# Optimization experiments

Measured on AMD Instinct MI355X. Metric: run time of the kernel, lower is better.

## Reference

```python
import jax, jax.numpy as jnp
import numpy as np

B, S, D, H, F = 4, 2048, 256, 8, 2  # batch, seq, input_size, heads, mlp factor
EPS = 1e-5


def _ln(x, g, b):
    m = jnp.mean(x, axis=-1, keepdims=True)
    v = jnp.var(x, axis=-1, keepdims=True)
    return (x - m) / jnp.sqrt(v + EPS) * g + b


def setup_inputs() -> dict:
    key = jax.random.key(0)
    ks = jax.random.split(key, 12)
    s = 1.0 / np.sqrt(D)
    return {
        "X":  jax.random.normal(ks[0], (B, S, D), jnp.float32),
        # Wide attention: each of H heads has full [D,D] Q/K/V projections (no bias)
        "Wq": jax.random.uniform(ks[1], (H, D, D), jnp.float32, -s, s),
        "Wk": jax.random.uniform(ks[2], (H, D, D), jnp.float32, -s, s),
        "Wv": jax.random.uniform(ks[3], (H, D, D), jnp.float32, -s, s),
        "Wz": jax.random.uniform(ks[4], (H * D, D), jnp.float32, -1.0 / np.sqrt(H * D), 1.0 / np.sqrt(H * D)),
        "bz": jnp.zeros((D,), jnp.float32),
        "W1": jax.random.uniform(ks[5], (D, F * D), jnp.float32, -s, s),
        "b1": jnp.zeros((F * D,), jnp.float32),
        "W2": jax.random.uniform(ks[6], (F * D, D), jnp.float32, -1.0 / np.sqrt(F * D), 1.0 / np.sqrt(F * D)),
        "b2": jnp.zeros((D,), jnp.float32),
        "g1": jnp.ones((D,), jnp.float32),
        "be1": jnp.zeros((D,), jnp.float32),
        "g2": jnp.ones((D,), jnp.float32),
        "be2": jnp.zeros((D,), jnp.float32),
    }


def reference(X, Wq, Wk, Wv, Wz, bz, W1, b1, W2, b2, g1, be1, g2, be2):
    scale = D ** (-0.25)  # applied to both q and k as in the source
    q = jnp.einsum('bsd,hde->hbse', X, Wq) * scale   # [H,B,S,D]
    k = jnp.einsum('btd,hde->hbte', X, Wk) * scale
    v = jnp.einsum('btd,hde->hbte', X, Wv)
    attn = jax.nn.softmax(jnp.einsum('hbse,hbte->hbst', q, k), axis=-1)  # [H,B,S,S]
    zh = jnp.einsum('hbst,hbte->hbse', attn, v)       # [H,B,S,D]
    # concat heads along feature dim (head order matters for Wz)
    zcat = jnp.transpose(zh, (1, 2, 0, 3)).reshape(B, S, H * D)
    z = zcat @ Wz + bz
    z = _ln(z + X, g1, be1)                            # dropout p=0 -> identity
    z_ff = jnp.maximum(z @ W1 + b1, 0.0) @ W2 + b2
    z = _ln(z_ff + z, g2, be2)
    attn_mean = jnp.mean(attn, axis=0)                 # [B,S,S]
    return z, attn_mean
```

## Files before the change

### kernel.cpp

```cpp
#include <hip/hip_runtime.h>
#include <cstdint>
#include <cstddef>

#define B_  4
#define S_  2048
#define D_  256
#define H_  8
#define FD_ 512
#define N_  (B_*S_)
#define HD_ (H_*D_)
#define EPS 1e-5f

typedef __attribute__((ext_vector_type(8))) short bf16x8;
typedef __attribute__((ext_vector_type(8))) unsigned short u16x8;
typedef __attribute__((ext_vector_type(4))) float f32x4;

__device__ __forceinline__ unsigned short f2bf(float f) {
  union { float f; unsigned u; } x; x.f = f;
  unsigned u = x.u;
  return (unsigned short)((u + 0x7FFFu + ((u >> 16) & 1u)) >> 16);
}
__device__ __forceinline__ float bf2f(unsigned short h) {
  union { unsigned u; float f; } x; x.u = ((unsigned)h) << 16; return x.f;
}

__device__ __forceinline__ void glds16(const void* gptr, void* ldsptr) {
  __builtin_amdgcn_global_load_lds(
      (__attribute__((address_space(1))) void*)gptr,
      (__attribute__((address_space(3))) void*)ldsptr,
      16, 0, 0);
}

__device__ __forceinline__ int sw32(int row, int u) {
  return (row*32 + ((u & 24) | ((u & 7) ^ (row & 7)))) * 8;
}
__device__ __forceinline__ int sw16(int row, int u) {
  return (row*16 + ((u & 8) | ((u & 7) ^ (row & 7)))) * 8;
}

__global__ __launch_bounds__(256) void cast_x_kernel(
    const float* __restrict__ X, unsigned short* __restrict__ Xb)
{
  const size_t i8 = ((size_t)blockIdx.x * 256 + threadIdx.x) * 8;
  float4 a = *(const float4*)&X[i8];
  float4 b = *(const float4*)&X[i8 + 4];
  u16x8 o;
  o[0]=f2bf(a.x); o[1]=f2bf(a.y); o[2]=f2bf(a.z); o[3]=f2bf(a.w);
  o[4]=f2bf(b.x); o[5]=f2bf(b.y); o[6]=f2bf(b.z); o[7]=f2bf(b.w);
  *(u16x8*)&Xb[i8] = o;
}

__global__ __launch_bounds__(256) void prep_w_kernel(
    const float* __restrict__ Wq, const float* __restrict__ Wk,
    const float* __restrict__ Wv, unsigned short* __restrict__ Wt)
{
  __shared__ float tile[64][65];
  const int tid = threadIdx.x;
  const int d0 = blockIdx.x * 64, e0 = blockIdx.y * 64;
  const int w = blockIdx.z;
  const float* src;
  float scale;
  if (w < 8)       { src = Wq + (size_t)w*D_*D_;      scale = 0.25f; }
  else if (w < 16) { src = Wk + (size_t)(w-8)*D_*D_;  scale = 0.25f; }
  else             { src = Wv + (size_t)(w-16)*D_*D_; scale = 1.0f;  }
  {
    int r = tid >> 2, c16 = (tid & 3) * 16;
    const float* s = src + (size_t)(d0 + r)*D_ + e0 + c16;
    #pragma unroll
    for (int u = 0; u < 4; ++u) *(float4*)&tile[r][c16 + u*4] = *(const float4*)(s + u*4);
  }
  __syncthreads();
  {
    int er = tid >> 2, dc = (tid & 3) * 16;
    u16x8 o0, o1;
    #pragma unroll
    for (int j = 0; j < 8; ++j) {
      o0[j] = f2bf(tile[dc + j][er] * scale);
      o1[j] = f2bf(tile[dc + 8 + j][er] * scale);
    }
    unsigned short* dst = Wt + ((size_t)w*D_ + e0 + er)*D_ + d0 + dc;
    *(u16x8*)(dst)     = o0;
    *(u16x8*)(dst + 8) = o1;
  }
}

__global__ __launch_bounds__(256) void tcast_kernel(
    const float* __restrict__ src, unsigned short* __restrict__ dst,
    int R, int C)
{
  __shared__ float tile[64][65];
  const int tid = threadIdx.x;
  const int r0 = blockIdx.x * 64, c0 = blockIdx.y * 64;
  {
    int r = tid >> 2, c16 = (tid & 3) * 16;
    const float* s = src + (size_t)(r0 + r)*C + c0 + c16;
    #pragma unroll
    for (int u = 0; u < 4; ++u) *(float4*)&tile[r][c16 + u*4] = *(const float4*)(s + u*4);
  }
  __syncthreads();
  {
    int cr = tid >> 2, rc = (tid & 3) * 16;
    u16x8 o0, o1;
    #pragma unroll
    for (int j = 0; j < 8; ++j) {
      o0[j] = f2bf(tile[rc + j][cr]);
      o1[j] = f2bf(tile[rc + 8 + j][cr]);
    }
    unsigned short* d = dst + (size_t)(c0 + cr)*R + r0 + rc;
    *(u16x8*)(d)     = o0;
    *(u16x8*)(d + 8) = o1;
  }
}

__global__ __launch_bounds__(256) void qkv_kernel(
    const unsigned short* __restrict__ Xb, const unsigned short* __restrict__ Wt,
    unsigned short* __restrict__ q, unsigned short* __restrict__ k,
    unsigned short* __restrict__ v)
{
  __shared__ unsigned short Xt[64*32*8];
  __shared__ unsigned short Wtile[64*32*8];
  const int tid = threadIdx.x;
  const int w4 = tid >> 6, lane = tid & 63;
  const int c = lane & 15, qd = lane >> 4;
  const int n0 = blockIdx.x * 64;
  const int e0 = blockIdx.y * 64;
  const int w  = blockIdx.z;

  unsigned short* obase;
  if (w < 8)       obase = q + (size_t)w*N_*D_;
  else if (w < 16) obase = k + (size_t)(w-8)*N_*D_;
  else             obase = v + (size_t)(w-16)*N_*D_;

  {
    const char* xg = (const char*)Xb + (size_t)n0*512;
    const char* wg = (const char*)Wt + ((size_t)w*D_ + e0)*512;
    #pragma unroll
    for (int i = 0; i < 8; ++i) {
      int g = w4*8 + i;
      int r = 2*g + (lane >> 5);
      int su = lane & 31;
      int u = (su & 24) | ((su & 7) ^ (r & 7));
      glds16(xg + (size_t)r*512 + u*16, &Xt[g*512]);
      glds16(wg + (size_t)r*512 + u*16, &Wtile[g*512]);
    }
  }
  __syncthreads();

  f32x4 sc[4];
  #pragma unroll
  for (int nc = 0; nc < 4; ++nc) sc[nc] = (f32x4){0.f,0.f,0.f,0.f};
  #pragma unroll
  for (int ks = 0; ks < 8; ++ks) {
    bf16x8 xa = *(const bf16x8*)&Xt[sw32(16*w4 + c, ks*4 + qd)];
    #pragma unroll
    for (int nc = 0; nc < 4; ++nc) {
      bf16x8 bf = *(const bf16x8*)&Wtile[sw32(nc*16 + c, ks*4 + qd)];
      sc[nc] = __builtin_amdgcn_mfma_f32_16x16x32_bf16(xa, bf, sc[nc], 0, 0, 0);
    }
  }
  #pragma unroll
  for (int nc = 0; nc < 4; ++nc)
    #pragma unroll
    for (int r = 0; r < 4; ++r)
      obase[(size_t)(n0 + 16*w4 + qd*4 + r)*D_ + e0 + nc*16 + c] = f2bf(sc[nc][r]);
}

__global__ __launch_bounds__(256) void vtrans_kernel(
    const unsigned short* __restrict__ vb, unsigned short* __restrict__ vT)
{
  __shared__ unsigned short tile[64][72];
  const int tid = threadIdx.x;
  const int t0 = blockIdx.x * 64, e0 = blockIdx.y * 64;
  const int h = blockIdx.z >> 2, b = blockIdx.z & 3;
  const size_t in_base = (size_t)h*N_*D_ + (size_t)b*S_*D_;
  {
    int r = tid >> 2, c16 = (tid & 3) * 16;
    const unsigned short* src = vb + in_base + (size_t)(t0 + r)*D_ + e0 + c16;
    *(u16x8*)&tile[r][c16]     = *(const u16x8*)(src);
    *(u16x8*)&tile[r][c16 + 8] = *(const u16x8*)(src + 8);
  }
  __syncthreads();
  {
    int er = tid >> 2, tt = (tid & 3) * 16;
    u16x8 o0, o1;
    #pragma unroll
    for (int j = 0; j < 8; ++j) { o0[j] = tile[tt+j][er]; o1[j] = tile[tt+8+j][er]; }
    unsigned short* dst = vT + ((size_t)(h*4 + b)*D_ + e0 + er)*S_ + t0 + tt;
    *(u16x8*)(dst)     = o0;
    *(u16x8*)(dst + 8) = o1;
  }
}

__global__ __launch_bounds__(256, 2) void attn_ol_kernel(
    const unsigned short* __restrict__ qb, const unsigned short* __restrict__ kb,
    const unsigned short* __restrict__ vT, unsigned short* __restrict__ zcatb,
    float* __restrict__ Lws)
{
  __shared__ unsigned short Kt[2][32*32*8];
  __shared__ unsigned short Vt[2][16*544];
  const int tid = threadIdx.x;
  const int w = tid >> 6, lane = tid & 63;
  const int c = lane & 15, qd = lane >> 4;
  const int s0 = blockIdx.x * 128;
  const int b = blockIdx.y, h = blockIdx.z;

  const size_t qkbase = (size_t)h*N_*D_ + (size_t)b*S_*D_;

  bf16x8 qa[2][8];
  #pragma unroll
  for (int mi = 0; mi < 2; ++mi) {
    const unsigned short* qrow = qb + qkbase + (size_t)(s0 + 32*w + 16*mi + c)*D_ + qd*8;
    #pragma unroll
    for (int ks = 0; ks < 8; ++ks) qa[mi][ks] = *(const bf16x8*)(qrow + ks*32);
  }

  f32x4 o[2][16];
  #pragma unroll
  for (int mi = 0; mi < 2; ++mi)
    #pragma unroll
    for (int i = 0; i < 16; ++i) o[mi][i] = (f32x4){0.f,0.f,0.f,0.f};
  float Lp[2] = {0.f, 0.f};

  const char* kB = (const char*)(kb + qkbase);
  const char* vB = (const char*)(vT + (size_t)(h*4 + b)*D_*S_);

  #define STAGE_OL(kt_, bi_)                                                   \
    {                                                                          \
      _Pragma("unroll")                                                        \
      for (int i = 0; i < 4; ++i) {                                            \
        int g = w*4 + i;                                                       \
        int r = 2*g + (lane >> 5);                                             \
        int Lg = ((r >> 2) & 3)*8 + (r >> 4)*4 + (r & 3);                      \
        int su = lane & 31;                                                    \
        int u = (su & 24) | ((su & 7) ^ (r & 7));                              \
        glds16(kB + ((size_t)(kt_)*32 + Lg)*512 + u*16, &Kt[bi_][g*512]);      \
      }                                                                        \
      _Pragma("unroll")                                                        \
      for (int i = 0; i < 4; ++i) {                                            \
        int g = w*4 + i;                                                       \
        int e = g*16 + (lane >> 2);                                            \
        int qv = (lane & 3) ^ ((lane >> 3) & 3);                               \
        glds16(vB + (size_t)e*4096 + (size_t)(kt_)*64 + qv*16, &Vt[bi_][g*544]);\
      }                                                                        \
    }

  STAGE_OL(0, 0);

  for (int kt = 0; kt < 64; ++kt) {
    const int bi = kt & 1;
    __syncthreads();
    if (kt + 1 < 64) STAGE_OL(kt + 1, bi ^ 1);

    f32x4 sc[2][2];
    #pragma unroll
    for (int mi = 0; mi < 2; ++mi)
      #pragma unroll
      for (int nc = 0; nc < 2; ++nc) sc[mi][nc] = (f32x4){0.f,0.f,0.f,0.f};
    #pragma unroll
    for (int ks = 0; ks < 8; ++ks) {
      bf16x8 kf0 = *(const bf16x8*)&Kt[bi][sw32(c,      ks*4 + qd)];
      bf16x8 kf1 = *(const bf16x8*)&Kt[bi][sw32(16 + c, ks*4 + qd)];
      #pragma unroll
      for (int mi = 0; mi < 2; ++mi) {
        sc[mi][0] = __builtin_amdgcn_mfma_f32_16x16x32_bf16(kf0, qa[mi][ks], sc[mi][0], 0, 0, 0);
        sc[mi][1] = __builtin_amdgcn_mfma_f32_16x16x32_bf16(kf1, qa[mi][ks], sc[mi][1], 0, 0, 0);
      }
    }
    bf16x8 pa[2];
    #pragma unroll
    for (int mi = 0; mi < 2; ++mi) {
      float ex[2][4];
      #pragma unroll
      for (int nc = 0; nc < 2; ++nc)
        #pragma unroll
        for (int r = 0; r < 4; ++r) {
          float p = __expf(sc[mi][nc][r]);
          ex[nc][r] = p;
          Lp[mi] += p;
        }
      union { unsigned u[4]; bf16x8 v; } cv;
      asm("v_cvt_pk_bf16_f32 %0, %1, %2" : "=v"(cv.u[0]) : "v"(ex[0][0]), "v"(ex[0][1]));
      asm("v_cvt_pk_bf16_f32 %0, %1, %2" : "=v"(cv.u[1]) : "v"(ex[0][2]), "v"(ex[0][3]));
      asm("v_cvt_pk_bf16_f32 %0, %1, %2" : "=v"(cv.u[2]) : "v"(ex[1][0]), "v"(ex[1][1]));
      asm("v_cvt_pk_bf16_f32 %0, %1, %2" : "=v"(cv.u[3]) : "v"(ex[1][2]), "v"(ex[1][3]));
      pa[mi] = cv.v;
    }
    #pragma unroll
    for (int ec = 0; ec < 16; ++ec) {
      bf16x8 vf = *(const bf16x8*)&Vt[bi][ec*544 + c*32 + (qd ^ ((c >> 1) & 3))*8];
      o[0][ec] = __builtin_amdgcn_mfma_f32_16x16x32_bf16(pa[0], vf, o[0][ec], 0, 0, 0);
      o[1][ec] = __builtin_amdgcn_mfma_f32_16x16x32_bf16(pa[1], vf, o[1][ec], 0, 0, 0);
    }
  }

  #pragma unroll
  for (int mi = 0; mi < 2; ++mi) {
    float L = Lp[mi];
    L += __shfl_xor(L, 16);
    L += __shfl_xor(L, 32);
    if (qd == 0)
      Lws[(size_t)h*N_ + b*S_ + s0 + 32*w + 16*mi + c] = L;
    float il[4];
    #pragma unroll
    for (int r = 0; r < 4; ++r)
      il[r] = 1.0f / __shfl(L, (lane & 48) | (qd*4 + r));
    #pragma unroll
    for (int ec = 0; ec < 16; ++ec)
      #pragma unroll
      for (int r = 0; r < 4; ++r)
        zcatb[(size_t)(b*S_ + s0 + 32*w + 16*mi + qd*4 + r)*HD_ + h*D_ + ec*16 + c] =
            f2bf(o[mi][ec][r] * il[r]);
  }
  #undef STAGE_OL
}

__global__ __launch_bounds__(256, 2) void attn_mean_kernel(
    const unsigned short* __restrict__ qb, const unsigned short* __restrict__ kb,
    const float* __restrict__ Lws, float* __restrict__ out_attn)
{
  __shared__ unsigned short Kt[2][64*32*8];
  const int tid = threadIdx.x;
  const int w = tid >> 6, lane = tid & 63;
  const int c = lane & 15, qd = lane >> 4;
  const int s0 = blockIdx.x * 128;
  const int t0 = blockIdx.y * 64;
  const int b = blockIdx.z;

  float am[2][4][4] = {};

  #define STAGE_AM(h_, bi_)                                                    \
    {                                                                          \
      const char* kB = (const char*)(kb + (size_t)(h_)*N_*D_ + (size_t)b*S_*D_);\
      _Pragma("unroll")                                                        \
      for (int i = 0; i < 8; ++i) {                                            \
        int g = w*8 + i;                                                       \
        int r = 2*g + (lane >> 5);                                             \
        int su = lane & 31;                                                    \
        int u = (su & 24) | ((su & 7) ^ (r & 7));                              \
        glds16(kB + ((size_t)t0 + r)*512 + u*16, &Kt[bi_][g*512]);             \
      }                                                                        \
    }

  STAGE_AM(0, 0);

  for (int h = 0; h < 8; ++h) {
    const int bi = h & 1;
    __syncthreads();
    if (h + 1 < 8) STAGE_AM(h + 1, bi ^ 1);

    const size_t base = (size_t)h*N_*D_ + (size_t)b*S_*D_;
    bf16x8 qa[2][8];
    #pragma unroll
    for (int mi = 0; mi < 2; ++mi) {
      const unsigned short* qrow = qb + base + (size_t)(s0 + 32*w + 16*mi + c)*D_ + qd*8;
      #pragma unroll
      for (int ks = 0; ks < 8; ++ks) qa[mi][ks] = *(const bf16x8*)(qrow + ks*32);
    }
    f32x4 sc[2][4];
    #pragma unroll
    for (int mi = 0; mi < 2; ++mi)
      #pragma unroll
      for (int nc = 0; nc < 4; ++nc) sc[mi][nc] = (f32x4){0.f,0.f,0.f,0.f};
    #pragma unroll
    for (int ks = 0; ks < 8; ++ks) {
      #pragma unroll
      for (int nc = 0; nc < 4; ++nc) {
        bf16x8 kf = *(const bf16x8*)&Kt[bi][sw32(nc*16 + c, ks*4 + qd)];
        sc[0][nc] = __builtin_amdgcn_mfma_f32_16x16x32_bf16(qa[0][ks], kf, sc[0][nc], 0, 0, 0);
        sc[1][nc] = __builtin_amdgcn_mfma_f32_16x16x32_bf16(qa[1][ks], kf, sc[1][nc], 0, 0, 0);
      }
    }
    #pragma unroll
    for (int mi = 0; mi < 2; ++mi) {
      float il8[4];
      #pragma unroll
      for (int r = 0; r < 4; ++r)
        il8[r] = 0.125f / Lws[(size_t)h*N_ + b*S_ + s0 + 32*w + 16*mi + qd*4 + r];
      #pragma unroll
      for (int nc = 0; nc < 4; ++nc)
        #pragma unroll
        for (int r = 0; r < 4; ++r)
          am[mi][nc][r] += __expf(sc[mi][nc][r]) * il8[r];
    }
  }
  #pragma unroll
  for (int mi = 0; mi < 2; ++mi)
    #pragma unroll
    for (int nc = 0; nc < 4; ++nc)
      #pragma unroll
      for (int r = 0; r < 4; ++r)
        out_attn[(size_t)(b*S_ + s0 + 32*w + 16*mi + qd*4 + r)*S_ + t0 + nc*16 + c] =
            am[mi][nc][r];
  #undef STAGE_AM
}

__global__ __launch_bounds__(256) void wz_ln1_kernel(
    const unsigned short* __restrict__ zcatb, const unsigned short* __restrict__ Wzt,
    const float* __restrict__ bz, const float* __restrict__ X,
    const float* __restrict__ g1, const float* __restrict__ be1,
    unsigned short* __restrict__ z1b)
{
  __shared__ unsigned short At[32*16*8];
  __shared__ unsigned short Wt2[256*16*8];
  __shared__ float redS[2][32], redQ[2][32];
  const int tid = threadIdx.x;
  const int w4 = tid >> 6, lane = tid & 63;
  const int c = lane & 15, qd = lane >> 4;
  const int n0 = blockIdx.x * 32;
  const int msub = w4 & 1, ehalf = w4 >> 1;

  f32x4 acc[8];
  #pragma unroll
  for (int nc = 0; nc < 8; ++nc) acc[nc] = (f32x4){0.f,0.f,0.f,0.f};

  for (int kc = 0; kc < 16; ++kc) {
    {
      const char* ab = (const char*)zcatb + (size_t)n0*4096 + (size_t)kc*256;
      #pragma unroll
      for (int i = 0; i < 2; ++i) {
        int g = w4*2 + i;
        int r = g*4 + (lane >> 4);
        int su = lane & 15;
        int u = (su & 8) | ((su & 7) ^ (r & 7));
        glds16(ab + (size_t)r*4096 + u*16, &At[g*512]);
      }
      const char* wb = (const char*)Wzt + (size_t)kc*256;
      #pragma unroll
      for (int i = 0; i < 16; ++i) {
        int g = w4*16 + i;
        int e = g*4 + (lane >> 4);
        int su = lane & 15;
        int u = (su & 8) | ((su & 7) ^ (e & 7));
        glds16(wb + (size_t)e*4096 + u*16, &Wt2[g*512]);
      }
    }
    __syncthreads();
    #pragma unroll
    for (int ks = 0; ks < 4; ++ks) {
      bf16x8 a = *(const bf16x8*)&At[sw16(msub*16 + c, ks*4 + qd)];
      #pragma unroll
      for (int nc = 0; nc < 8; ++nc) {
        bf16x8 bv = *(const bf16x8*)&Wt2[sw16(ehalf*128 + nc*16 + c, ks*4 + qd)];
        acc[nc] = __builtin_amdgcn_mfma_f32_16x16x32_bf16(a, bv, acc[nc], 0, 0, 0);
      }
    }
    __syncthreads();
  }

  float vals[8][4];
  float sum_[4] = {0.f,0.f,0.f,0.f}, sq_[4] = {0.f,0.f,0.f,0.f};
  #pragma unroll
  for (int nc = 0; nc < 8; ++nc) {
    int e = ehalf*128 + nc*16 + c;
    #pragma unroll
    for (int r = 0; r < 4; ++r) {
      int n = n0 + msub*16 + qd*4 + r;
      float v = acc[nc][r] + bz[e] + X[(size_t)n*D_ + e];
      vals[nc][r] = v;
      sum_[r] += v; sq_[r] += v*v;
    }
  }
  #pragma unroll
  for (int off = 1; off < 16; off <<= 1) {
    #pragma unroll
    for (int r = 0; r < 4; ++r) {
      sum_[r] += __shfl_xor(sum_[r], off);
      sq_[r]  += __shfl_xor(sq_[r],  off);
    }
  }
  if (c == 0) {
    #pragma unroll
    for (int r = 0; r < 4; ++r) {
      redS[ehalf][msub*16 + qd*4 + r] = sum_[r];
      redQ[ehalf][msub*16 + qd*4 + r] = sq_[r];
    }
  }
  __syncthreads();
  #pragma unroll
  for (int r = 0; r < 4; ++r) {
    int lr = msub*16 + qd*4 + r;
    float Sv = redS[0][lr] + redS[1][lr];
    float Qv = redQ[0][lr] + redQ[1][lr];
    float mean = Sv * (1.0f/D_);
    float var  = Qv * (1.0f/D_) - mean*mean;
    float rstd = rsqrtf(var + EPS);
    int n = n0 + lr;
    #pragma unroll
    for (int nc = 0; nc < 8; ++nc) {
      int e = ehalf*128 + nc*16 + c;
      z1b[(size_t)n*D_ + e] = f2bf((vals[nc][r] - mean)*rstd*g1[e] + be1[e]);
    }
  }
}

__global__ __launch_bounds__(256) void mlp1_kernel(
    const unsigned short* __restrict__ z1b, const unsigned short* __restrict__ W1t,
    const float* __restrict__ b1, unsigned short* __restrict__ hbuf)
{
  __shared__ unsigned short At[64*32*8];
  __shared__ unsigned short Bt[64*32*8];
  const int tid = threadIdx.x;
  const int w4 = tid >> 6, lane = tid & 63;
  const int c = lane & 15, qd = lane >> 4;
  const int n0 = blockIdx.x * 64;
  const int f0 = blockIdx.y * 64;

  {
    const char* ag = (const char*)z1b + (size_t)n0*512;
    const char* bg = (const char*)W1t + (size_t)f0*512;
    #pragma unroll
    for (int i = 0; i < 8; ++i) {
      int g = w4*8 + i;
      int r = 2*g + (lane >> 5);
      int su = lane & 31;
      int u = (su & 24) | ((su & 7) ^ (r & 7));
      glds16(ag + (size_t)r*512 + u*16, &At[g*512]);
      glds16(bg + (size_t)r*512 + u*16, &Bt[g*512]);
    }
  }
  __syncthreads();

  f32x4 sc[4];
  #pragma unroll
  for (int nc = 0; nc < 4; ++nc) sc[nc] = (f32x4){0.f,0.f,0.f,0.f};
  #pragma unroll
  for (int ks = 0; ks < 8; ++ks) {
    bf16x8 xa = *(const bf16x8*)&At[sw32(16*w4 + c, ks*4 + qd)];
    #pragma unroll
    for (int nc = 0; nc < 4; ++nc) {
      bf16x8 bf = *(const bf16x8*)&Bt[sw32(nc*16 + c, ks*4 + qd)];
      sc[nc] = __builtin_amdgcn_mfma_f32_16x16x32_bf16(xa, bf, sc[nc], 0, 0, 0);
    }
  }
  #pragma unroll
  for (int nc = 0; nc < 4; ++nc) {
    int f = f0 + nc*16 + c;
    float bias = b1[f];
    #pragma unroll
    for (int r = 0; r < 4; ++r)
      hbuf[(size_t)(n0 + 16*w4 + qd*4 + r)*FD_ + f] = f2bf(fmaxf(sc[nc][r] + bias, 0.f));
  }
}

__global__ __launch_bounds__(256) void mlp2_kernel(
    const unsigned short* __restrict__ hbuf, const unsigned short* __restrict__ W2t,
    const float* __restrict__ b2, const unsigned short* __restrict__ z1b,
    const float* __restrict__ g2, const float* __restrict__ be2,
    float* __restrict__ out)
{
  __shared__ unsigned short At[32*16*8];
  __shared__ unsigned short Wt2[256*16*8];
  __shared__ float redS[2][32], redQ[2][32];
  const int tid = threadIdx.x;
  const int w4 = tid >> 6, lane = tid & 63;
  const int c = lane & 15, qd = lane >> 4;
  const int n0 = blockIdx.x * 32;
  const int msub = w4 & 1, ehalf = w4 >> 1;

  f32x4 acc[8];
  #pragma unroll
  for (int nc = 0; nc < 8; ++nc) acc[nc] = (f32x4){0.f,0.f,0.f,0.f};

  for (int kc = 0; kc < 4; ++kc) {
    {
      const char* ab = (const char*)hbuf + (size_t)n0*1024 + (size_t)kc*256;
      #pragma unroll
      for (int i = 0; i < 2; ++i) {
        int g = w4*2 + i;
        int r = g*4 + (lane >> 4);
        int su = lane & 15;
        int u = (su & 8) | ((su & 7) ^ (r & 7));
        glds16(ab + (size_t)r*1024 + u*16, &At[g*512]);
      }
      const char* wb = (const char*)W2t + (size_t)kc*256;
      #pragma unroll
      for (int i = 0; i < 16; ++i) {
        int g = w4*16 + i;
        int e = g*4 + (lane >> 4);
        int su = lane & 15;
        int u = (su & 8) | ((su & 7) ^ (e & 7));
        glds16(wb + (size_t)e*1024 + u*16, &Wt2[g*512]);
      }
    }
    __syncthreads();
    #pragma unroll
    for (int ks = 0; ks < 4; ++ks) {
      bf16x8 a = *(const bf16x8*)&At[sw16(msub*16 + c, ks*4 + qd)];
      #pragma unroll
      for (int nc = 0; nc < 8; ++nc) {
        bf16x8 bv = *(const bf16x8*)&Wt2[sw16(ehalf*128 + nc*16 + c, ks*4 + qd)];
        acc[nc] = __builtin_amdgcn_mfma_f32_16x16x32_bf16(a, bv, acc[nc], 0, 0, 0);
      }
    }
    __syncthreads();
  }

  float vals[8][4];
  float sum_[4] = {0.f,0.f,0.f,0.f}, sq_[4] = {0.f,0.f,0.f,0.f};
  #pragma unroll
  for (int nc = 0; nc < 8; ++nc) {
    int e = ehalf*128 + nc*16 + c;
    #pragma unroll
    for (int r = 0; r < 4; ++r) {
      int n = n0 + msub*16 + qd*4 + r;
      float v = acc[nc][r] + b2[e] + bf2f(z1b[(size_t)n*D_ + e]);
      vals[nc][r] = v;
      sum_[r] += v; sq_[r] += v*v;
    }
  }
  #pragma unroll
  for (int off = 1; off < 16; off <<= 1) {
    #pragma unroll
    for (int r = 0; r < 4; ++r) {
      sum_[r] += __shfl_xor(sum_[r], off);
      sq_[r]  += __shfl_xor(sq_[r],  off);
    }
  }
  if (c == 0) {
    #pragma unroll
    for (int r = 0; r < 4; ++r) {
      redS[ehalf][msub*16 + qd*4 + r] = sum_[r];
      redQ[ehalf][msub*16 + qd*4 + r] = sq_[r];
    }
  }
  __syncthreads();
  #pragma unroll
  for (int r = 0; r < 4; ++r) {
    int lr = msub*16 + qd*4 + r;
    float Sv = redS[0][lr] + redS[1][lr];
    float Qv = redQ[0][lr] + redQ[1][lr];
    float mean = Sv * (1.0f/D_);
    float var  = Qv * (1.0f/D_) - mean*mean;
    float rstd = rsqrtf(var + EPS);
    int n = n0 + lr;
    #pragma unroll
    for (int nc = 0; nc < 8; ++nc) {
      int e = ehalf*128 + nc*16 + c;
      out[(size_t)n*D_ + e] = (vals[nc][r] - mean)*rstd*g2[e] + be2[e];
    }
  }
}

extern "C" void kernel_launch(void* const* d_in, const int* in_sizes, int n_in,
                              void* d_out, int out_size, void* d_ws, size_t ws_size,
                              hipStream_t stream)
{
  (void)in_sizes; (void)n_in; (void)out_size; (void)ws_size;
  const float* X   = (const float*)d_in[0];
  const float* Wq  = (const float*)d_in[1];
  const float* Wk  = (const float*)d_in[2];
  const float* Wv  = (const float*)d_in[3];
  const float* Wz  = (const float*)d_in[4];
  const float* bz  = (const float*)d_in[5];
  const float* W1  = (const float*)d_in[6];
  const float* b1  = (const float*)d_in[7];
  const float* W2  = (const float*)d_in[8];
  const float* b2  = (const float*)d_in[9];
  const float* g1  = (const float*)d_in[10];
  const float* be1 = (const float*)d_in[11];
  const float* g2  = (const float*)d_in[12];
  const float* be2 = (const float*)d_in[13];

  char* p = (char*)d_ws;
  unsigned short* Xbb  = (unsigned short*)p; p += (size_t)N_*D_*2;
  unsigned short* Wtb  = (unsigned short*)p; p += (size_t)24*D_*D_*2;
  unsigned short* Wztb = (unsigned short*)p; p += (size_t)D_*HD_*2;
  unsigned short* W1tb = (unsigned short*)p; p += (size_t)FD_*D_*2;
  unsigned short* W2tb = (unsigned short*)p; p += (size_t)D_*FD_*2;
  unsigned short* qbuf = (unsigned short*)p; p += (size_t)H_*N_*D_*2;
  unsigned short* kbuf = (unsigned short*)p; p += (size_t)H_*N_*D_*2;
  unsigned short* vbuf = (unsigned short*)p; p += (size_t)H_*N_*D_*2;
  unsigned short* vTb  = (unsigned short*)p; p += (size_t)H_*N_*D_*2;
  float* Lws   = (float*)p; p += (size_t)H_*N_*4;
  unsigned short* zcatb = (unsigned short*)p; p += (size_t)N_*HD_*2;
  unsigned short* z1b   = (unsigned short*)p; p += (size_t)N_*D_*2;
  unsigned short* hbuf  = (unsigned short*)p;

  float* out_z    = (float*)d_out;
  float* out_attn = out_z + (size_t)N_*D_;

  cast_x_kernel<<<N_*D_/(256*8), 256, 0, stream>>>(X, Xbb);

  dim3 gW(4, 4, 24);
  prep_w_kernel<<<gW, 256, 0, stream>>>(Wq, Wk, Wv, Wtb);

  { dim3 g(HD_/64, D_/64);  tcast_kernel<<<g, 256, 0, stream>>>(Wz, Wztb, HD_, D_); }
  { dim3 g(D_/64, FD_/64);  tcast_kernel<<<g, 256, 0, stream>>>(W1, W1tb, D_, FD_); }
  { dim3 g(FD_/64, D_/64);  tcast_kernel<<<g, 256, 0, stream>>>(W2, W2tb, FD_, D_); }

  dim3 gA(N_/64, D_/64, 24);
  qkv_kernel<<<gA, 256, 0, stream>>>(Xbb, Wtb, qbuf, kbuf, vbuf);

  dim3 gT(S_/64, D_/64, H_*B_);
  vtrans_kernel<<<gT, 256, 0, stream>>>(vbuf, vTb);

  dim3 gB1(S_/128, B_, H_);
  attn_ol_kernel<<<gB1, 256, 0, stream>>>(qbuf, kbuf, vTb, zcatb, Lws);

  dim3 gB2(S_/128, S_/64, B_);
  attn_mean_kernel<<<gB2, 256, 0, stream>>>(qbuf, kbuf, Lws, out_attn);

  wz_ln1_kernel<<<N_/32, 256, 0, stream>>>(zcatb, Wztb, bz, X, g1, be1, z1b);

  dim3 gM1(N_/64, FD_/64);
  mlp1_kernel<<<gM1, 256, 0, stream>>>(z1b, W1tb, b1, hbuf);

  mlp2_kernel<<<N_/32, 256, 0, stream>>>(hbuf, W2tb, b2, z1b, g2, be2, out_z);
}
```

Before: 536.0 us.

## Store softmax probabilities from the attention kernel instead of recomputing QK^T for the head mean

The attention kernel now writes its unnormalized bf16 exp(QK^T) tiles to a workspace buffer. A new simple reduction kernel then scales each head's tile by 0.125/L and sums them into the head-mean attention output. This replaces the old attn_mean kernel, which recomputed every head's QK^T with MFMA and re-evaluated the exponentials. Heads are processed in chunks sized to the available workspace, so the old compute is traded for a large amount of extra HBM write and read traffic. The mean is also now built from bf16-rounded probabilities rather than fp32 ones, which slightly lowers its precision.

```diff
diff --git a/kernel.cpp b/kernel.cpp
--- a/kernel.cpp
+++ b/kernel.cpp
@@ -194,7 +194,7 @@
 __global__ __launch_bounds__(256, 2) void attn_ol_kernel(
     const unsigned short* __restrict__ qb, const unsigned short* __restrict__ kb,
     const unsigned short* __restrict__ vT, unsigned short* __restrict__ zcatb,
-    float* __restrict__ Lws)
+    float* __restrict__ Lws, unsigned short* __restrict__ Pout, int hbase)
 {
   __shared__ unsigned short Kt[2][32*32*8];
   __shared__ unsigned short Vt[2][16*544];
@@ -202,7 +202,9 @@
   const int w = tid >> 6, lane = tid & 63;
   const int c = lane & 15, qd = lane >> 4;
   const int s0 = blockIdx.x * 128;
-  const int b = blockIdx.y, h = blockIdx.z;
+  const int b = blockIdx.y;
+  const int hz = blockIdx.z;
+  const int h = hbase + hz;
 
   const size_t qkbase = (size_t)h*N_*D_ + (size_t)b*S_*D_;
 
@@ -223,6 +225,9 @@
 
   const char* kB = (const char*)(kb + qkbase);
   const char* vB = (const char*)(vT + (size_t)(h*4 + b)*D_*S_);
+
+  unsigned short* Pb0 = Pout + ((size_t)hz*N_ + (size_t)b*S_ + s0 + 32*w + c)*S_ + qd*8;
+  unsigned short* Pb1 = Pb0 + (size_t)16*S_;
 
   #define STAGE_OL(kt_, bi_)                                                   \
     {                                                                          \
@@ -285,6 +290,8 @@
       asm("v_cvt_pk_bf16_f32 %0, %1, %2" : "=v"(cv.u[3]) : "v"(ex[1][2]), "v"(ex[1][3]));
       pa[mi] = cv.v;
     }
+    *(bf16x8*)(Pb0 + (size_t)kt*32) = pa[0];
+    *(bf16x8*)(Pb1 + (size_t)kt*32) = pa[1];
     #pragma unroll
     for (int ec = 0; ec < 16; ++ec) {
       bf16x8 vf = *(const bf16x8*)&Vt[bi][ec*544 + c*32 + (qd ^ ((c >> 1) & 3))*8];
@@ -314,84 +321,32 @@
   #undef STAGE_OL
 }
 
-__global__ __launch_bounds__(256, 2) void attn_mean_kernel(
-    const unsigned short* __restrict__ qb, const unsigned short* __restrict__ kb,
-    const float* __restrict__ Lws, float* __restrict__ out_attn)
-{
-  __shared__ unsigned short Kt[2][64*32*8];
-  const int tid = threadIdx.x;
-  const int w = tid >> 6, lane = tid & 63;
-  const int c = lane & 15, qd = lane >> 4;
-  const int s0 = blockIdx.x * 128;
-  const int t0 = blockIdx.y * 64;
-  const int b = blockIdx.z;
-
-  float am[2][4][4] = {};
-
-  #define STAGE_AM(h_, bi_)                                                    \
-    {                                                                          \
-      const char* kB = (const char*)(kb + (size_t)(h_)*N_*D_ + (size_t)b*S_*D_);\
-      _Pragma("unroll")                                                        \
-      for (int i = 0; i < 8; ++i) {                                            \
-        int g = w*8 + i;                                                       \
-        int r = 2*g + (lane >> 5);                                             \
-        int su = lane & 31;                                                    \
-        int u = (su & 24) | ((su & 7) ^ (r & 7));                              \
-        glds16(kB + ((size_t)t0 + r)*512 + u*16, &Kt[bi_][g*512]);             \
-      }                                                                        \
-    }
-
-  STAGE_AM(0, 0);
-
-  for (int h = 0; h < 8; ++h) {
-    const int bi = h & 1;
-    __syncthreads();
-    if (h + 1 < 8) STAGE_AM(h + 1, bi ^ 1);
-
-    const size_t base = (size_t)h*N_*D_ + (size_t)b*S_*D_;
-    bf16x8 qa[2][8];
-    #pragma unroll
-    for (int mi = 0; mi < 2; ++mi) {
-      const unsigned short* qrow = qb + base + (size_t)(s0 + 32*w + 16*mi + c)*D_ + qd*8;
-      #pragma unroll
-      for (int ks = 0; ks < 8; ++ks) qa[mi][ks] = *(const bf16x8*)(qrow + ks*32);
-    }
-    f32x4 sc[2][4];
-    #pragma unroll
-    for (int mi = 0; mi < 2; ++mi)
-      #pragma unroll
-      for (int nc = 0; nc < 4; ++nc) sc[mi][nc] = (f32x4){0.f,0.f,0.f,0.f};
-    #pragma unroll
-    for (int ks = 0; ks < 8; ++ks) {
-      #pragma unroll
-      for (int nc = 0; nc < 4; ++nc) {
-        bf16x8 kf = *(const bf16x8*)&Kt[bi][sw32(nc*16 + c, ks*4 + qd)];
-        sc[0][nc] = __builtin_amdgcn_mfma_f32_16x16x32_bf16(qa[0][ks], kf, sc[0][nc], 0, 0, 0);
-        sc[1][nc] = __builtin_amdgcn_mfma_f32_16x16x32_bf16(qa[1][ks], kf, sc[1][nc], 0, 0, 0);
-      }
-    }
-    #pragma unroll
-    for (int mi = 0; mi < 2; ++mi) {
-      float il8[4];
-      #pragma unroll
-      for (int r = 0; r < 4; ++r)
-        il8[r] = 0.125f / Lws[(size_t)h*N_ + b*S_ + s0 + 32*w + 16*mi + qd*4 + r];
-      #pragma unroll
-      for (int nc = 0; nc < 4; ++nc)
-        #pragma unroll
-        for (int r = 0; r < 4; ++r)
-          am[mi][nc][r] += __expf(sc[mi][nc][r]) * il8[r];
-    }
-  }
-  #pragma unroll
-  for (int mi = 0; mi < 2; ++mi)
-    #pragma unroll
-    for (int nc = 0; nc < 4; ++nc)
-      #pragma unroll
-      for (int r = 0; r < 4; ++r)
-        out_attn[(size_t)(b*S_ + s0 + 32*w + 16*mi + qd*4 + r)*S_ + t0 + nc*16 + c] =
-            am[mi][nc][r];
-  #undef STAGE_AM
+__global__ __launch_bounds__(256) void attn_mean_kernel(
+    const unsigned short* __restrict__ P, const float* __restrict__ Lws,
+    float* __restrict__ out_attn, int hbase, int hcount)
+{
+  const int n = blockIdx.x;
+  const int t0 = threadIdx.x * 8;
+  float acc[8];
+  if (hbase == 0) {
+    #pragma unroll
+    for (int j = 0; j < 8; ++j) acc[j] = 0.f;
+  } else {
+    float4 a = *(const float4*)&out_attn[(size_t)n*S_ + t0];
+    float4 b = *(const float4*)&out_attn[(size_t)n*S_ + t0 + 4];
+    acc[0]=a.x; acc[1]=a.y; acc[2]=a.z; acc[3]=a.w;
+    acc[4]=b.x; acc[5]=b.y; acc[6]=b.z; acc[7]=b.w;
+  }
+  for (int hz = 0; hz < hcount; ++hz) {
+    float il = 0.125f / Lws[(size_t)(hbase + hz)*N_ + n];
+    u16x8 pv = *(const u16x8*)&P[((size_t)hz*N_ + n)*S_ + t0];
+    #pragma unroll
+    for (int j = 0; j < 8; ++j) acc[j] += bf2f(pv[j]) * il;
+  }
+  float4 o0 = {acc[0], acc[1], acc[2], acc[3]};
+  float4 o1 = {acc[4], acc[5], acc[6], acc[7]};
+  *(float4*)&out_attn[(size_t)n*S_ + t0]     = o0;
+  *(float4*)&out_attn[(size_t)n*S_ + t0 + 4] = o1;
 }
 
 __global__ __launch_bounds__(256) void wz_ln1_kernel(
@@ -645,7 +600,7 @@
                               void* d_out, int out_size, void* d_ws, size_t ws_size,
                               hipStream_t stream)
 {
-  (void)in_sizes; (void)n_in; (void)out_size; (void)ws_size;
+  (void)in_sizes; (void)n_in; (void)out_size;
   const float* X   = (const float*)d_in[0];
   const float* Wq  = (const float*)d_in[1];
   const float* Wk  = (const float*)d_in[2];
@@ -661,20 +616,39 @@
   const float* g2  = (const float*)d_in[12];
   const float* be2 = (const float*)d_in[13];
 
+  const size_t SZ_XB = (size_t)N_*D_*2;
+  const size_t SZ_WT = (size_t)24*D_*D_*2;
+  const size_t SZ_WZ = (size_t)D_*HD_*2;
+  const size_t SZ_W1 = (size_t)FD_*D_*2;
+  const size_t SZ_W2 = (size_t)D_*FD_*2;
+  const size_t SZ_QK = (size_t)H_*N_*D_*2;
+  const size_t SZ_L  = (size_t)H_*N_*4;
+  const size_t SZ_ZC = (size_t)N_*HD_*2;
+  const size_t SZ_Z1 = (size_t)N_*D_*2;
+  const size_t SZ_PH = (size_t)N_*S_*2;
+
   char* p = (char*)d_ws;
-  unsigned short* Xbb  = (unsigned short*)p; p += (size_t)N_*D_*2;
-  unsigned short* Wtb  = (unsigned short*)p; p += (size_t)24*D_*D_*2;
-  unsigned short* Wztb = (unsigned short*)p; p += (size_t)D_*HD_*2;
-  unsigned short* W1tb = (unsigned short*)p; p += (size_t)FD_*D_*2;
-  unsigned short* W2tb = (unsigned short*)p; p += (size_t)D_*FD_*2;
-  unsigned short* qbuf = (unsigned short*)p; p += (size_t)H_*N_*D_*2;
-  unsigned short* kbuf = (unsigned short*)p; p += (size_t)H_*N_*D_*2;
-  unsigned short* vbuf = (unsigned short*)p; p += (size_t)H_*N_*D_*2;
-  unsigned short* vTb  = (unsigned short*)p; p += (size_t)H_*N_*D_*2;
-  float* Lws   = (float*)p; p += (size_t)H_*N_*4;
-  unsigned short* zcatb = (unsigned short*)p; p += (size_t)N_*HD_*2;
-  unsigned short* z1b   = (unsigned short*)p; p += (size_t)N_*D_*2;
-  unsigned short* hbuf  = (unsigned short*)p;
+  unsigned short* Xbb  = (unsigned short*)p; p += SZ_XB;
+  unsigned short* Wtb  = (unsigned short*)p; p += SZ_WT;
+  unsigned short* Wztb = (unsigned short*)p; p += SZ_WZ;
+  unsigned short* W1tb = (unsigned short*)p; p += SZ_W1;
+  unsigned short* W2tb = (unsigned short*)p; p += SZ_W2;
+  unsigned short* qbuf = (unsigned short*)p; p += SZ_QK;
+  unsigned short* kbuf = (unsigned short*)p; p += SZ_QK;
+  unsigned short* vTb  = (unsigned short*)p; p += SZ_QK;
+  float* Lws   = (float*)p; p += SZ_L;
+  unsigned short* zcatb = (unsigned short*)p; p += SZ_ZC;
+  unsigned short* z1b   = (unsigned short*)p; p += SZ_Z1;
+  char* shared = p;
+  const size_t fixed_sz = (size_t)(shared - (char*)d_ws);
+  unsigned short* vbuf = (unsigned short*)shared;
+  unsigned short* Pbuf = (unsigned short*)shared;
+  unsigned short* hbuf = (unsigned short*)shared;
+
+  int hcount = 1;
+  if      (fixed_sz + 8*SZ_PH <= ws_size) hcount = 8;
+  else if (fixed_sz + 4*SZ_PH <= ws_size) hcount = 4;
+  else if (fixed_sz + 2*SZ_PH <= ws_size) hcount = 2;
 
   float* out_z    = (float*)d_out;
   float* out_attn = out_z + (size_t)N_*D_;
@@ -694,11 +668,11 @@
   dim3 gT(S_/64, D_/64, H_*B_);
   vtrans_kernel<<<gT, 256, 0, stream>>>(vbuf, vTb);
 
-  dim3 gB1(S_/128, B_, H_);
-  attn_ol_kernel<<<gB1, 256, 0, stream>>>(qbuf, kbuf, vTb, zcatb, Lws);
-
-  dim3 gB2(S_/128, S_/64, B_);
-  attn_mean_kernel<<<gB2, 256, 0, stream>>>(qbuf, kbuf, Lws, out_attn);
+  for (int hb = 0; hb < H_; hb += hcount) {
+    dim3 gB1(S_/128, B_, hcount);
+    attn_ol_kernel<<<gB1, 256, 0, stream>>>(qbuf, kbuf, vTb, zcatb, Lws, Pbuf, hb);
+    attn_mean_kernel<<<N_, 256, 0, stream>>>(Pbuf, Lws, out_attn, hb, hcount);
+  }
 
   wz_ln1_kernel<<<N_/32, 256, 0, stream>>>(zcatb, Wztb, bz, X, g1, be1, z1b);
 
```

Result: slower. 639.5 us (+19.3%).

## Remap attention grids to XCD-aware 1D order and prefetch next head's Q

Applied to the files above, without the earlier changes.

Both attention kernels now use a flat 1D grid whose block index is decoded so that blocks sharing the same K/V head-batch stream land on the same XCD (round-robin dispatch by wg&7). The intent is to improve L2 reuse of K and V tiles within each XCD's private cache. The attn_mean kernel also software-prefetches the next head's Q fragments into registers during the current head's MFMA work and hoists the L-normalisation loads ahead of the MFMAs. The prefetch raises register pressure and could affect occupancy under the two-blocks-per-CU launch bound.

```diff
diff --git a/kernel.cpp b/kernel.cpp
--- a/kernel.cpp
+++ b/kernel.cpp
@@ -201,8 +201,14 @@
   const int tid = threadIdx.x;
   const int w = tid >> 6, lane = tid & 63;
   const int c = lane & 15, qd = lane >> 4;
-  const int s0 = blockIdx.x * 128;
-  const int b = blockIdx.y, h = blockIdx.z;
+  const int wg = blockIdx.x;
+  const int xcd = wg & 7;
+  const int slot = wg >> 3;
+  const int j = slot & 15;
+  const int gg = slot >> 4;
+  const int g = gg*8 + xcd;
+  const int h = g >> 2, b = g & 3;
+  const int s0 = j * 128;
 
   const size_t qkbase = (size_t)h*N_*D_ + (size_t)b*S_*D_;
 
@@ -228,19 +234,19 @@
     {                                                                          \
       _Pragma("unroll")                                                        \
       for (int i = 0; i < 4; ++i) {                                            \
-        int g = w*4 + i;                                                       \
-        int r = 2*g + (lane >> 5);                                             \
+        int gq = w*4 + i;                                                      \
+        int r = 2*gq + (lane >> 5);                                            \
         int Lg = ((r >> 2) & 3)*8 + (r >> 4)*4 + (r & 3);                      \
         int su = lane & 31;                                                    \
         int u = (su & 24) | ((su & 7) ^ (r & 7));                              \
-        glds16(kB + ((size_t)(kt_)*32 + Lg)*512 + u*16, &Kt[bi_][g*512]);      \
+        glds16(kB + ((size_t)(kt_)*32 + Lg)*512 + u*16, &Kt[bi_][gq*512]);     \
       }                                                                        \
       _Pragma("unroll")                                                        \
       for (int i = 0; i < 4; ++i) {                                            \
-        int g = w*4 + i;                                                       \
-        int e = g*16 + (lane >> 2);                                            \
+        int gq = w*4 + i;                                                      \
+        int e = gq*16 + (lane >> 2);                                           \
         int qv = (lane & 3) ^ ((lane >> 3) & 3);                               \
-        glds16(vB + (size_t)e*4096 + (size_t)(kt_)*64 + qv*16, &Vt[bi_][g*544]);\
+        glds16(vB + (size_t)e*4096 + (size_t)(kt_)*64 + qv*16, &Vt[bi_][gq*544]);\
       }                                                                        \
     }
 
@@ -322,9 +328,15 @@
   const int tid = threadIdx.x;
   const int w = tid >> 6, lane = tid & 63;
   const int c = lane & 15, qd = lane >> 4;
-  const int s0 = blockIdx.x * 128;
-  const int t0 = blockIdx.y * 64;
-  const int b = blockIdx.z;
+  const int wg = blockIdx.x;
+  const int xcd = wg & 7;
+  const int slot = wg >> 3;
+  const int j = slot & 15;
+  const int ggg = slot >> 4;
+  const int g = ggg*8 + xcd;
+  const int b = g >> 5;
+  const int t0 = (g & 31) * 64;
+  const int s0 = j * 128;
 
   float am[2][4][4] = {};
 
@@ -333,29 +345,47 @@
       const char* kB = (const char*)(kb + (size_t)(h_)*N_*D_ + (size_t)b*S_*D_);\
       _Pragma("unroll")                                                        \
       for (int i = 0; i < 8; ++i) {                                            \
-        int g = w*8 + i;                                                       \
-        int r = 2*g + (lane >> 5);                                             \
+        int gq = w*8 + i;                                                      \
+        int r = 2*gq + (lane >> 5);                                            \
         int su = lane & 31;                                                    \
         int u = (su & 24) | ((su & 7) ^ (r & 7));                              \
-        glds16(kB + ((size_t)t0 + r)*512 + u*16, &Kt[bi_][g*512]);             \
+        glds16(kB + ((size_t)t0 + r)*512 + u*16, &Kt[bi_][gq*512]);            \
       }                                                                        \
     }
 
   STAGE_AM(0, 0);
+
+  bf16x8 qa[2][8];
+  #pragma unroll
+  for (int mi = 0; mi < 2; ++mi) {
+    const unsigned short* qrow = qb + (size_t)b*S_*D_ + (size_t)(s0 + 32*w + 16*mi + c)*D_ + qd*8;
+    #pragma unroll
+    for (int ks = 0; ks < 8; ++ks) qa[mi][ks] = *(const bf16x8*)(qrow + ks*32);
+  }
 
   for (int h = 0; h < 8; ++h) {
     const int bi = h & 1;
     __syncthreads();
     if (h + 1 < 8) STAGE_AM(h + 1, bi ^ 1);
 
-    const size_t base = (size_t)h*N_*D_ + (size_t)b*S_*D_;
-    bf16x8 qa[2][8];
-    #pragma unroll
-    for (int mi = 0; mi < 2; ++mi) {
-      const unsigned short* qrow = qb + base + (size_t)(s0 + 32*w + 16*mi + c)*D_ + qd*8;
-      #pragma unroll
-      for (int ks = 0; ks < 8; ++ks) qa[mi][ks] = *(const bf16x8*)(qrow + ks*32);
-    }
+    float il[2][4];
+    #pragma unroll
+    for (int mi = 0; mi < 2; ++mi)
+      #pragma unroll
+      for (int r = 0; r < 4; ++r)
+        il[mi][r] = 0.125f / Lws[(size_t)h*N_ + b*S_ + s0 + 32*w + 16*mi + qd*4 + r];
+
+    bf16x8 qn[2][8];
+    if (h + 1 < 8) {
+      const size_t basen = (size_t)(h+1)*N_*D_ + (size_t)b*S_*D_;
+      #pragma unroll
+      for (int mi = 0; mi < 2; ++mi) {
+        const unsigned short* qrow = qb + basen + (size_t)(s0 + 32*w + 16*mi + c)*D_ + qd*8;
+        #pragma unroll
+        for (int ks = 0; ks < 8; ++ks) qn[mi][ks] = *(const bf16x8*)(qrow + ks*32);
+      }
+    }
+
     f32x4 sc[2][4];
     #pragma unroll
     for (int mi = 0; mi < 2; ++mi)
@@ -371,16 +401,18 @@
       }
     }
     #pragma unroll
-    for (int mi = 0; mi < 2; ++mi) {
-      float il8[4];
-      #pragma unroll
-      for (int r = 0; r < 4; ++r)
-        il8[r] = 0.125f / Lws[(size_t)h*N_ + b*S_ + s0 + 32*w + 16*mi + qd*4 + r];
+    for (int mi = 0; mi < 2; ++mi)
       #pragma unroll
       for (int nc = 0; nc < 4; ++nc)
         #pragma unroll
         for (int r = 0; r < 4; ++r)
-          am[mi][nc][r] += __expf(sc[mi][nc][r]) * il8[r];
+          am[mi][nc][r] += __expf(sc[mi][nc][r]) * il[mi][r];
+
+    if (h + 1 < 8) {
+      #pragma unroll
+      for (int mi = 0; mi < 2; ++mi)
+        #pragma unroll
+        for (int ks = 0; ks < 8; ++ks) qa[mi][ks] = qn[mi][ks];
     }
   }
   #pragma unroll
@@ -694,11 +726,9 @@
   dim3 gT(S_/64, D_/64, H_*B_);
   vtrans_kernel<<<gT, 256, 0, stream>>>(vbuf, vTb);
 
-  dim3 gB1(S_/128, B_, H_);
-  attn_ol_kernel<<<gB1, 256, 0, stream>>>(qbuf, kbuf, vTb, zcatb, Lws);
-
-  dim3 gB2(S_/128, S_/64, B_);
-  attn_mean_kernel<<<gB2, 256, 0, stream>>>(qbuf, kbuf, Lws, out_attn);
+  attn_ol_kernel<<<512, 256, 0, stream>>>(qbuf, kbuf, vTb, zcatb, Lws);
+
+  attn_mean_kernel<<<2048, 256, 0, stream>>>(qbuf, kbuf, Lws, out_attn);
 
   wz_ln1_kernel<<<N_/32, 256, 0, stream>>>(zcatb, Wztb, bz, X, g1, be1, z1b);
 
```

Result: no change. 533.8 us (-0.4%).
